# Kernel tuning notes

Measured on AMD Instinct MI355X. Metric: run time of the kernel, lower is better.

## Reference

```python
import jax, jax.numpy as jnp
import numpy as np

B, N, DIM = 2, 2048, 1024
H, DH = 16, 64
INNER = H * DH
SCALE = DH ** -0.5


def rotate_half(x):
    x1, x2 = jnp.split(x, 2, axis=-1)
    return jnp.concatenate((-x2, x1), axis=-1)


def apply_rotary(pos, t):
    # pos: [n, dh] broadcast against t: [b, h, n, dh]
    return t * jnp.cos(pos) + rotate_half(t) * jnp.sin(pos)


def setup_inputs() -> dict:
    key = jax.random.key(0)
    ks = jax.random.split(key, 5)
    x = jax.random.normal(ks[0], (B, N, DIM), dtype=jnp.float32)
    rotary_emb = jax.random.normal(ks[1], (N, DH), dtype=jnp.float32)
    w_qkv = jax.random.normal(ks[2], (3 * INNER, DIM), dtype=jnp.float32) * (DIM ** -0.5)
    w_out = jax.random.normal(ks[3], (DIM, INNER), dtype=jnp.float32) * (INNER ** -0.5)
    b_out = jax.random.normal(ks[4], (DIM,), dtype=jnp.float32) * 0.01
    return {"x": x, "rotary_emb": rotary_emb, "w_qkv": w_qkv, "w_out": w_out, "b_out": b_out}


def reference(x, rotary_emb, w_qkv, w_out, b_out):
    b, n, _ = x.shape
    qkv = jnp.einsum('bnd,ed->bne', x, w_qkv)  # [b, n, 3*inner]
    q, k, v = jnp.split(qkv, 3, axis=-1)
    # [b, n, inner] -> [b, h, n, dh]
    reshape = lambda t: t.reshape(b, n, H, DH).transpose(0, 2, 1, 3)
    q, k, v = reshape(q), reshape(k), reshape(v)
    q = apply_rotary(rotary_emb, q)
    k = apply_rotary(rotary_emb, k)
    dots = jnp.einsum('bhid,bhjd->bhij', q, k) * SCALE
    attn = jax.nn.softmax(dots, axis=-1)
    out = jnp.einsum('bhij,bhjd->bhid', attn, v)
    out = out.transpose(0, 2, 1, 3).reshape(b, n, INNER)
    return jnp.einsum('bne,de->bnd', out, w_out) + b_out
```

## Files before the change

### kernel.cpp

```cpp
#include <hip/hip_runtime.h>
#include <math.h>

typedef unsigned short ushort_t;
typedef __attribute__((ext_vector_type(8))) short short8v;
typedef __attribute__((ext_vector_type(4))) float float4v;

#define BB 2
#define NN 2048
#define HH 16
#define DHH 64
#define DIMM 1024
#define QKV3 3072
#define INNERR 1024
#define QSCALE 0.1803368801111244f

__device__ __forceinline__ ushort_t f2bf(float f) {
    unsigned u = __float_as_uint(f);
    u += 0x7fffu + ((u >> 16) & 1u);
    return (ushort_t)(u >> 16);
}
__device__ __forceinline__ float bf2f(unsigned h) {
    return __uint_as_float(h << 16);
}
__device__ __forceinline__ unsigned pk_bf16(float a, float b) {
#if __has_builtin(__builtin_amdgcn_cvt_pk_bf16_f32)
    typedef __attribute__((ext_vector_type(2))) __bf16 bf16x2;
    bf16x2 r = __builtin_amdgcn_cvt_pk_bf16_f32(a, b);
    return __builtin_bit_cast(unsigned, r);
#else
    return (unsigned)f2bf(a) | ((unsigned)f2bf(b) << 16);
#endif
}
__device__ __forceinline__ float fast_exp2(float x) {
#if __has_builtin(__builtin_amdgcn_exp2f)
    return __builtin_amdgcn_exp2f(x);
#else
    return exp2f(x);
#endif
}
__device__ __forceinline__ void gl2lds16(const void* g, void* l) {
    __builtin_amdgcn_global_load_lds(
        (const __attribute__((address_space(1))) unsigned int*)g,
        (__attribute__((address_space(3))) unsigned int*)l, 16, 0, 0);
}

__global__ __launch_bounds__(256) void conv_fused(const float* __restrict__ x,
                                                  const float* __restrict__ wqkv,
                                                  const float* __restrict__ wout,
                                                  ushort_t* __restrict__ xo,
                                                  ushort_t* __restrict__ wqkvo,
                                                  ushort_t* __restrict__ wouto) {
    int blk = blockIdx.x;
    const float* in; ushort_t* out; int i;
    if (blk < 4096)      { in = x;    out = xo;    i = blk * 256 + threadIdx.x; }
    else if (blk < 7168) { in = wqkv; out = wqkvo; i = (blk - 4096) * 256 + threadIdx.x; }
    else                 { in = wout; out = wouto; i = (blk - 7168) * 256 + threadIdx.x; }
    float4 v = ((const float4*)in)[i];
    ushort4 o;
    o.x = f2bf(v.x); o.y = f2bf(v.y); o.z = f2bf(v.z); o.w = f2bf(v.w);
    ((ushort4*)out)[i] = o;
}

template <int NOUT, bool BF16OUT, bool BIAS, bool ROT>
__global__ __launch_bounds__(256, 6) void gemm_bf16(const ushort_t* __restrict__ A,
                                                    const ushort_t* __restrict__ Bm,
                                                    const float* __restrict__ bias,
                                                    const float* __restrict__ rot,
                                                    ushort_t* __restrict__ Vt,
                                                    void* __restrict__ Cout, int K) {
    constexpr int NCH = 3;
    __shared__ ushort_t As[2][128 * 32];
    __shared__ ushort_t Bs[2][64 * 32];
    const int t = threadIdx.x;
    const int lane = t & 63;
    const int w = t >> 6;
    const int quad = lane >> 4;
    const int l15 = lane & 15;
    const int m0 = blockIdx.y * 128;
    const int n0 = blockIdx.x * 64;
    const int wm = w * 32;

    float4v acc[2][4];
#pragma unroll
    for (int i = 0; i < 2; ++i)
#pragma unroll
        for (int j = 0; j < 4; ++j) acc[i][j] = (float4v)0.0f;

    int srow[NCH], slc[NCH], sdst[NCH];
    bool sisA[NCH];
#pragma unroll
    for (int u = 0; u < NCH; ++u) {
        int c = u * 256 + t;
        if (c < 512) {
            int row = c >> 2;
            sisA[u] = true; srow[u] = row; slc[u] = (c & 3) ^ ((row >> 1) & 3); sdst[u] = c * 8;
        } else {
            int cb = c - 512;
            int row = cb >> 2;
            sisA[u] = false; srow[u] = row; slc[u] = (cb & 3) ^ ((row >> 1) & 3); sdst[u] = cb * 8;
        }
    }
#pragma unroll
    for (int u = 0; u < NCH; ++u) {
        if (sisA[u]) gl2lds16(&A[(size_t)(m0 + srow[u]) * K + slc[u] * 8], &As[0][sdst[u]]);
        else         gl2lds16(&Bm[(size_t)(n0 + srow[u]) * K + slc[u] * 8], &Bs[0][sdst[u]]);
    }
    const int NIT = K >> 5;
    for (int it = 0; it < NIT; ++it) {
        const int cur = it & 1;
        if (it + 1 < NIT) {
            const int nxt = cur ^ 1;
            const int kc = (it + 1) << 5;
#pragma unroll
            for (int u = 0; u < NCH; ++u) {
                if (sisA[u]) gl2lds16(&A[(size_t)(m0 + srow[u]) * K + kc + slc[u] * 8], &As[nxt][sdst[u]]);
                else         gl2lds16(&Bm[(size_t)(n0 + srow[u]) * K + kc + slc[u] * 8], &Bs[nxt][sdst[u]]);
            }
            asm volatile("s_waitcnt vmcnt(3)\n\ts_barrier" ::: "memory");
        } else {
            asm volatile("s_waitcnt vmcnt(0)\n\ts_barrier" ::: "memory");
        }
        short8v a[2], b[4];
#pragma unroll
        for (int i = 0; i < 2; ++i) {
            int row = wm + i * 16 + l15;
            int pc = quad ^ ((row >> 1) & 3);
            a[i] = *(const short8v*)&As[cur][row * 32 + pc * 8];
        }
#pragma unroll
        for (int j = 0; j < 4; ++j) {
            int row = j * 16 + l15;
            int pc = quad ^ ((row >> 1) & 3);
            b[j] = *(const short8v*)&Bs[cur][row * 32 + pc * 8];
        }
#pragma unroll
        for (int i = 0; i < 2; ++i)
#pragma unroll
            for (int j = 0; j < 4; ++j)
                acc[i][j] = __builtin_amdgcn_mfma_f32_16x16x32_bf16(a[i], b[j], acc[i][j], 0, 0, 0);
        asm volatile("s_barrier" ::: "memory");
    }
    const int region = ROT ? (n0 >> 10) : 0;
    if (ROT && region == 2) {
#pragma unroll
        for (int i = 0; i < 2; ++i) {
            int grow = m0 + wm + i * 16 + quad * 4;
            int bb = grow >> 11, nn_ = grow & (NN - 1);
            int tk = nn_ & 63;
            int tp = (tk & 32) | ((tk & 12) << 1) | ((tk & 16) >> 2);
            int nstore = (nn_ & ~63) | tp;
#pragma unroll
            for (int j = 0; j < 4; ++j) {
                int vcol = n0 + j * 16 + l15 - 2048;
                int hh = vcol >> 6, dh = vcol & 63;
                uint2 st;
                st.x = pk_bf16(acc[i][j][0], acc[i][j][1]);
                st.y = pk_bf16(acc[i][j][2], acc[i][j][3]);
                *(uint2*)&Vt[((size_t)(bb * HH + hh) * DHH + dh) * NN + nstore] = st;
            }
        }
        return;
    }
    if (ROT) {
        float scale = (region == 0) ? QSCALE : 1.0f;
#pragma unroll
        for (int i = 0; i < 2; ++i) {
#pragma unroll
            for (int r = 0; r < 4; ++r) {
                int n = (m0 + wm + i * 16 + quad * 4 + r) & (NN - 1);
#pragma unroll
                for (int jl = 0; jl < 2; ++jl) {
                    int dh = jl * 16 + l15;
                    float plo = rot[n * DHH + dh];
                    float phi = rot[n * DHH + dh + 32];
                    float lo = acc[i][jl][r], hi = acc[i][jl + 2][r];
                    acc[i][jl][r]     = (lo * __cosf(plo) - hi * __sinf(plo)) * scale;
                    acc[i][jl + 2][r] = (hi * __cosf(phi) + lo * __sinf(phi)) * scale;
                }
            }
        }
    }
#pragma unroll
    for (int i = 0; i < 2; ++i) {
        int grow = m0 + wm + i * 16 + quad * 4;
#pragma unroll
        for (int j = 0; j < 4; ++j) {
            int gcol = n0 + j * 16 + l15;
            float bv = BIAS ? bias[gcol] : 0.0f;
#pragma unroll
            for (int r = 0; r < 4; ++r) {
                float v = acc[i][j][r] + bv;
                if (BF16OUT)
                    ((ushort_t*)Cout)[(size_t)(grow + r) * NOUT + gcol] = f2bf(v);
                else
                    ((float*)Cout)[(size_t)(grow + r) * NOUT + gcol] = v;
            }
        }
    }
}

__global__ __launch_bounds__(256, 4) void flash_mfma(const ushort_t* __restrict__ qkv,
                                                     const ushort_t* __restrict__ Vt,
                                                     ushort_t* __restrict__ po,
                                                     float* __restrict__ lp) {
    __shared__ ushort_t smem[16384];
    ushort_t* Osc = smem;
    const int t = threadIdx.x;
    const int lane = t & 63;
    const int w = t >> 6;
    const int quad = lane >> 4;
    const int l15 = lane & 15;
    const int blk = blockIdx.x;
    const int slot = blk >> 3;
    const int ks = slot & 1;
    const int qt = (slot >> 1) & 15;
    const int bh = (blk & 7) * 4 + (slot >> 5);
    const int b = bh >> 4, h = bh & 15;
    const int n0 = qt * 128;

    short8v bq[2][2];
#pragma unroll
    for (int g = 0; g < 2; ++g) {
        size_t qb = (size_t)(b * NN + n0 + w * 32 + g * 16 + l15) * QKV3 + h * DHH + quad * 8;
        bq[g][0] = *(const short8v*)&qkv[qb];
        bq[g][1] = *(const short8v*)&qkv[qb + 32];
    }
    float4v o_acc[2][4];
    float4v l_acc[2];
#pragma unroll
    for (int g = 0; g < 2; ++g) {
        l_acc[g] = (float4v)0.0f;
#pragma unroll
        for (int nb = 0; nb < 4; ++nb) o_acc[g][nb] = (float4v)0.0f;
    }
    const short one_bf = (short)0x3F80;
    short8v ones8 = {one_bf, one_bf, one_bf, one_bf, one_bf, one_bf, one_bf, one_bf};

    const int s0 = t, s1 = 256 + t;
    const int r0 = s0 >> 3, lc0 = (s0 & 7) ^ (r0 & 7);
    const int r1 = s1 >> 3, lc1 = (s1 & 7) ^ (r1 & 7);
    const int koff0 = r0 * QKV3 + lc0 * 8, koff1 = r1 * QKV3 + lc1 * 8;
    const int voff0 = r0 * NN + lc0 * 8,   voff1 = r1 * NN + lc1 * 8;
    const ushort_t* kp = qkv + (size_t)b * NN * QKV3 + INNERR + h * DHH + (size_t)ks * 1024 * QKV3;
    const ushort_t* vp = Vt + (size_t)(b * HH + h) * DHH * NN + ks * 1024;

    {
        gl2lds16(kp + koff0, smem + 0 * 4096 + s0 * 8);
        gl2lds16(kp + koff1, smem + 0 * 4096 + s1 * 8);
        gl2lds16(vp + voff0, smem + 2 * 4096 + s0 * 8);
        gl2lds16(vp + voff1, smem + 2 * 4096 + s1 * 8);
    }
    for (int jt = 0; jt < 16; ++jt) {
        const int cur = jt & 1;
        if (jt < 15) {
            kp += 64 * QKV3;
            vp += 64;
            const int nxt = cur ^ 1;
            gl2lds16(kp + koff0, smem + nxt * 4096 + s0 * 8);
            gl2lds16(kp + koff1, smem + nxt * 4096 + s1 * 8);
            gl2lds16(vp + voff0, smem + (2 + nxt) * 4096 + s0 * 8);
            gl2lds16(vp + voff1, smem + (2 + nxt) * 4096 + s1 * 8);
            asm volatile("s_waitcnt vmcnt(4)\n\ts_barrier" ::: "memory");
        } else {
            asm volatile("s_waitcnt vmcnt(0)\n\ts_barrier" ::: "memory");
        }
        const ushort_t* Ksc = smem + cur * 4096;
        const ushort_t* Vtc = smem + (2 + cur) * 4096;
        float4v s_acc[2][4];
#pragma unroll
        for (int g = 0; g < 2; ++g)
#pragma unroll
            for (int nb = 0; nb < 4; ++nb) s_acc[g][nb] = (float4v)0.0f;
#pragma unroll
        for (int kb = 0; kb < 2; ++kb)
#pragma unroll
            for (int nb = 0; nb < 4; ++nb) {
                int row = nb * 16 + l15;
                int pc = (kb * 4 + quad) ^ (row & 7);
                short8v ak = *(const short8v*)&Ksc[row * 64 + pc * 8];
                s_acc[0][nb] = __builtin_amdgcn_mfma_f32_16x16x32_bf16(ak, bq[0][kb], s_acc[0][nb], 0, 0, 0);
                s_acc[1][nb] = __builtin_amdgcn_mfma_f32_16x16x32_bf16(ak, bq[1][kb], s_acc[1][nb], 0, 0, 0);
            }
#pragma unroll
        for (int g = 0; g < 2; ++g) {
            float p[4][4];
#pragma unroll
            for (int nb = 0; nb < 4; ++nb)
#pragma unroll
                for (int r = 0; r < 4; ++r) p[nb][r] = fast_exp2(s_acc[g][nb][r]);
            uint4 u0, u1;
            u0.x = pk_bf16(p[0][0], p[0][1]); u0.y = pk_bf16(p[0][2], p[0][3]);
            u0.z = pk_bf16(p[1][0], p[1][1]); u0.w = pk_bf16(p[1][2], p[1][3]);
            u1.x = pk_bf16(p[2][0], p[2][1]); u1.y = pk_bf16(p[2][2], p[2][3]);
            u1.z = pk_bf16(p[3][0], p[3][1]); u1.w = pk_bf16(p[3][2], p[3][3]);
            short8v ap0 = __builtin_bit_cast(short8v, u0);
            short8v ap1 = __builtin_bit_cast(short8v, u1);
            l_acc[g] = __builtin_amdgcn_mfma_f32_16x16x32_bf16(ap0, ones8, l_acc[g], 0, 0, 0);
            l_acc[g] = __builtin_amdgcn_mfma_f32_16x16x32_bf16(ap1, ones8, l_acc[g], 0, 0, 0);
#pragma unroll
            for (int nb = 0; nb < 4; ++nb) {
                int row = nb * 16 + l15;
                int pc0 = quad ^ (row & 7);
                int pc1 = (4 + quad) ^ (row & 7);
                short8v bv0 = *(const short8v*)&Vtc[row * 64 + pc0 * 8];
                short8v bv1 = *(const short8v*)&Vtc[row * 64 + pc1 * 8];
                o_acc[g][nb] = __builtin_amdgcn_mfma_f32_16x16x32_bf16(ap0, bv0, o_acc[g][nb], 0, 0, 0);
                o_acc[g][nb] = __builtin_amdgcn_mfma_f32_16x16x32_bf16(ap1, bv1, o_acc[g][nb], 0, 0, 0);
            }
        }
        asm volatile("s_barrier" ::: "memory");
    }
#pragma unroll
    for (int g = 0; g < 2; ++g) {
        if (l15 == 0)
            *(float4*)&lp[(size_t)(ks * 32 + bh) * NN + n0 + w * 32 + g * 16 + quad * 4] =
                *(float4*)&l_acc[g];
    }
    ushort_t* osc = Osc + w * (32 * 68);
#pragma unroll
    for (int g = 0; g < 2; ++g)
#pragma unroll
        for (int nb = 0; nb < 4; ++nb)
#pragma unroll
            for (int r = 0; r < 4; ++r)
                osc[(g * 16 + quad * 4 + r) * 68 + nb * 16 + l15] = f2bf(o_acc[g][nb][r]);
    __builtin_amdgcn_s_waitcnt(0);
    {
        int rr = lane >> 1, c0 = (lane & 1) * 32;
        size_t prow = ((size_t)(ks * 32 + bh) * NN + n0 + w * 32 + rr) * DHH + c0;
#pragma unroll
        for (int u = 0; u < 4; ++u) {
            uint4 v = *(const uint4*)&osc[rr * 68 + c0 + u * 8];
            *(uint4*)&po[prow + u * 8] = v;
        }
    }
}

__global__ __launch_bounds__(256) void reduce_o(const ushort_t* __restrict__ po,
                                                const float* __restrict__ lp,
                                                ushort_t* __restrict__ attn) {
    int tg = blockIdx.x * 256 + threadIdx.x;
    int bh = tg >> 15;
    int rem = tg & 32767;
    int n = rem >> 4;
    int dh0 = (rem & 15) * 4;
    size_t p0 = ((size_t)bh * NN + n) * DHH + dh0;
    size_t p1 = p0 + (size_t)32 * NN * DHH;
    uint2 a = *(const uint2*)&po[p0];
    uint2 c = *(const uint2*)&po[p1];
    float inv = 1.0f / (lp[(size_t)bh * NN + n] + lp[(size_t)(32 + bh) * NN + n]);
    float o0 = (bf2f(a.x & 0xffff) + bf2f(c.x & 0xffff)) * inv;
    float o1 = (bf2f(a.x >> 16)    + bf2f(c.x >> 16))    * inv;
    float o2 = (bf2f(a.y & 0xffff) + bf2f(c.y & 0xffff)) * inv;
    float o3 = (bf2f(a.y >> 16)    + bf2f(c.y >> 16))    * inv;
    int b = bh >> 4, h = bh & 15;
    uint2 st;
    st.x = pk_bf16(o0, o1);
    st.y = pk_bf16(o2, o3);
    *(uint2*)&attn[((size_t)(b * NN + n)) * INNERR + h * DHH + dh0] = st;
}

extern "C" void kernel_launch(void* const* d_in, const int* in_sizes, int n_in,
                              void* d_out, int out_size, void* d_ws, size_t ws_size,
                              hipStream_t stream) {
    const float* x = (const float*)d_in[0];
    const float* rot = (const float*)d_in[1];
    const float* w_qkv = (const float*)d_in[2];
    const float* w_out = (const float*)d_in[3];
    const float* b_out = (const float*)d_in[4];
    float* y = (float*)d_out;

    char* ws = (char*)d_ws;
    ushort_t* qkv_bf  = (ushort_t*)(ws);
    ushort_t* vt_bf   = (ushort_t*)(ws + 25165824);
    ushort_t* wout_bf = (ushort_t*)(ws + 33554432);
    ushort_t* wqkv_bf = (ushort_t*)(ws + 35651584);
    float*    lp      = (float*)(ws + 35651584);
    ushort_t* x_bf    = (ushort_t*)(ws + 41943040);
    ushort_t* attn_bf = x_bf;
    ushort_t* po      = (ushort_t*)(ws + 50331648);

    conv_fused<<<8192, 256, 0, stream>>>(x, w_qkv, w_out, x_bf, wqkv_bf, wout_bf);
    gemm_bf16<QKV3, true, false, true><<<dim3(48, 32), 256, 0, stream>>>(
        x_bf, wqkv_bf, nullptr, rot, vt_bf, qkv_bf, DIMM);
    flash_mfma<<<1024, 256, 0, stream>>>(qkv_bf, vt_bf, po, lp);
    reduce_o<<<4096, 256, 0, stream>>>(po, lp, attn_bf);
    gemm_bf16<INNERR, false, true, false><<<dim3(16, 32), 256, 0, stream>>>(
        attn_bf, wout_bf, b_out, nullptr, nullptr, y, INNERR);
}
```

Measured before the change: 201.3 us.

## Add block-index swizzle and smaller 64-row tile for output projection GEMM

Makes the GEMM template take the tile height and a swizzle width. The grid becomes 1D, and block indices are remapped so that groups of blocks share N tiles, which is meant to improve L2 reuse. The output projection now uses 64x64 tiles with a 2x2 warp layout, giving 1024 blocks instead of 512 for better occupancy across CUs. The cost is smaller per-block MFMA work and more redundant A/B loads for that GEMM.

After: 202.4 us. About the same (+0.6%).

```diff
diff --git a/kernel.cpp b/kernel.cpp
--- a/kernel.cpp
+++ b/kernel.cpp
@@ -61,41 +61,46 @@
     ((ushort4*)out)[i] = o;
 }
 
-template <int NOUT, bool BF16OUT, bool BIAS, bool ROT>
+template <int NOUT, bool BF16OUT, bool BIAS, bool ROT, int BM, int SWXN>
 __global__ __launch_bounds__(256, 6) void gemm_bf16(const ushort_t* __restrict__ A,
                                                     const ushort_t* __restrict__ Bm,
                                                     const float* __restrict__ bias,
                                                     const float* __restrict__ rot,
                                                     ushort_t* __restrict__ Vt,
                                                     void* __restrict__ Cout, int K) {
-    constexpr int NCH = 3;
-    __shared__ ushort_t As[2][128 * 32];
+    constexpr int JN = (BM == 128) ? 4 : 2;
+    constexpr int ACH = BM * 4;
+    constexpr int NCH = (ACH + 256) / 256;
+    __shared__ ushort_t As[2][BM * 32];
     __shared__ ushort_t Bs[2][64 * 32];
     const int t = threadIdx.x;
     const int lane = t & 63;
     const int w = t >> 6;
     const int quad = lane >> 4;
     const int l15 = lane & 15;
-    const int m0 = blockIdx.y * 128;
-    const int n0 = blockIdx.x * 64;
-    const int wm = w * 32;
-
-    float4v acc[2][4];
+    const int blk = blockIdx.x;
+    const int ii = blk >> 3;
+    const int m0 = (ii / SWXN) * BM;
+    const int n0 = ((blk & 7) * SWXN + ii % SWXN) * 64;
+    const int wm = (BM == 128) ? w * 32 : (w >> 1) * 32;
+    const int wn = (BM == 128) ? 0 : (w & 1) * 32;
+
+    float4v acc[2][JN];
 #pragma unroll
     for (int i = 0; i < 2; ++i)
 #pragma unroll
-        for (int j = 0; j < 4; ++j) acc[i][j] = (float4v)0.0f;
+        for (int j = 0; j < JN; ++j) acc[i][j] = (float4v)0.0f;
 
     int srow[NCH], slc[NCH], sdst[NCH];
     bool sisA[NCH];
 #pragma unroll
     for (int u = 0; u < NCH; ++u) {
         int c = u * 256 + t;
-        if (c < 512) {
+        if (c < ACH) {
             int row = c >> 2;
             sisA[u] = true; srow[u] = row; slc[u] = (c & 3) ^ ((row >> 1) & 3); sdst[u] = c * 8;
         } else {
-            int cb = c - 512;
+            int cb = c - ACH;
             int row = cb >> 2;
             sisA[u] = false; srow[u] = row; slc[u] = (cb & 3) ^ ((row >> 1) & 3); sdst[u] = cb * 8;
         }
@@ -116,11 +121,12 @@
                 if (sisA[u]) gl2lds16(&A[(size_t)(m0 + srow[u]) * K + kc + slc[u] * 8], &As[nxt][sdst[u]]);
                 else         gl2lds16(&Bm[(size_t)(n0 + srow[u]) * K + kc + slc[u] * 8], &Bs[nxt][sdst[u]]);
             }
-            asm volatile("s_waitcnt vmcnt(3)\n\ts_barrier" ::: "memory");
+            if (NCH == 3) asm volatile("s_waitcnt vmcnt(3)\n\ts_barrier" ::: "memory");
+            else          asm volatile("s_waitcnt vmcnt(2)\n\ts_barrier" ::: "memory");
         } else {
             asm volatile("s_waitcnt vmcnt(0)\n\ts_barrier" ::: "memory");
         }
-        short8v a[2], b[4];
+        short8v a[2], b[JN];
 #pragma unroll
         for (int i = 0; i < 2; ++i) {
             int row = wm + i * 16 + l15;
@@ -128,15 +134,15 @@
             a[i] = *(const short8v*)&As[cur][row * 32 + pc * 8];
         }
 #pragma unroll
-        for (int j = 0; j < 4; ++j) {
-            int row = j * 16 + l15;
+        for (int j = 0; j < JN; ++j) {
+            int row = wn + j * 16 + l15;
             int pc = quad ^ ((row >> 1) & 3);
             b[j] = *(const short8v*)&Bs[cur][row * 32 + pc * 8];
         }
 #pragma unroll
         for (int i = 0; i < 2; ++i)
 #pragma unroll
-            for (int j = 0; j < 4; ++j)
+            for (int j = 0; j < JN; ++j)
                 acc[i][j] = __builtin_amdgcn_mfma_f32_16x16x32_bf16(a[i], b[j], acc[i][j], 0, 0, 0);
         asm volatile("s_barrier" ::: "memory");
     }
@@ -150,7 +156,7 @@
             int tp = (tk & 32) | ((tk & 12) << 1) | ((tk & 16) >> 2);
             int nstore = (nn_ & ~63) | tp;
 #pragma unroll
-            for (int j = 0; j < 4; ++j) {
+            for (int j = 0; j < JN; ++j) {
                 int vcol = n0 + j * 16 + l15 - 2048;
                 int hh = vcol >> 6, dh = vcol & 63;
                 uint2 st;
@@ -184,8 +190,8 @@
     for (int i = 0; i < 2; ++i) {
         int grow = m0 + wm + i * 16 + quad * 4;
 #pragma unroll
-        for (int j = 0; j < 4; ++j) {
-            int gcol = n0 + j * 16 + l15;
+        for (int j = 0; j < JN; ++j) {
+            int gcol = n0 + wn + j * 16 + l15;
             float bv = BIAS ? bias[gcol] : 0.0f;
 #pragma unroll
             for (int r = 0; r < 4; ++r) {
@@ -381,10 +387,10 @@
     ushort_t* po      = (ushort_t*)(ws + 50331648);
 
     conv_fused<<<8192, 256, 0, stream>>>(x, w_qkv, w_out, x_bf, wqkv_bf, wout_bf);
-    gemm_bf16<QKV3, true, false, true><<<dim3(48, 32), 256, 0, stream>>>(
+    gemm_bf16<QKV3, true, false, true, 128, 6><<<1536, 256, 0, stream>>>(
         x_bf, wqkv_bf, nullptr, rot, vt_bf, qkv_bf, DIMM);
     flash_mfma<<<1024, 256, 0, stream>>>(qkv_bf, vt_bf, po, lp);
     reduce_o<<<4096, 256, 0, stream>>>(po, lp, attn_bf);
-    gemm_bf16<INNERR, false, true, false><<<dim3(16, 32), 256, 0, stream>>>(
+    gemm_bf16<INNERR, false, true, false, 64, 2><<<1024, 256, 0, stream>>>(
         attn_bf, wout_bf, b_out, nullptr, nullptr, y, INNERR);
 }
```

## Fuse split-KV reduction into output GEMM and remap block tiles

Applied to the files above, without the earlier changes.

Removes the separate reduce_o kernel by having a new output-projection GEMM load both split-KV partial outputs and row sums, then normalize and convert them to bf16 while staging A tiles into shared memory. The output GEMM also moves to 64x64 tiles with 1024 blocks instead of 128x64 with 512 blocks. The QKV GEMM becomes a specialized kernel with a 1D grid that groups blocks across N columns, aiming for better L2 reuse. This saves one launch and an intermediate write and read, but adds redundant reduction work, since each A element is recombined for every N-tile, and uses a smaller tile for the final GEMM.

New measurement: 209.0 us. 3.9% more time.

```diff
diff --git a/kernel.cpp b/kernel.cpp
--- a/kernel.cpp
+++ b/kernel.cpp
@@ -61,13 +61,13 @@
     ((ushort4*)out)[i] = o;
 }
 
-template <int NOUT, bool BF16OUT, bool BIAS, bool ROT>
-__global__ __launch_bounds__(256, 6) void gemm_bf16(const ushort_t* __restrict__ A,
+template <int SWXN>
+__global__ __launch_bounds__(256, 6) void gemm1_qkv(const ushort_t* __restrict__ A,
                                                     const ushort_t* __restrict__ Bm,
-                                                    const float* __restrict__ bias,
                                                     const float* __restrict__ rot,
                                                     ushort_t* __restrict__ Vt,
-                                                    void* __restrict__ Cout, int K) {
+                                                    ushort_t* __restrict__ Cout) {
+    constexpr int K = DIMM;
     constexpr int NCH = 3;
     __shared__ ushort_t As[2][128 * 32];
     __shared__ ushort_t Bs[2][64 * 32];
@@ -76,8 +76,10 @@
     const int w = t >> 6;
     const int quad = lane >> 4;
     const int l15 = lane & 15;
-    const int m0 = blockIdx.y * 128;
-    const int n0 = blockIdx.x * 64;
+    const int blk = blockIdx.x;
+    const int ii = blk >> 3;
+    const int m0 = (ii / SWXN) * 128;
+    const int n0 = ((blk & 7) * SWXN + ii % SWXN) * 64;
     const int wm = w * 32;
 
     float4v acc[2][4];
@@ -140,8 +142,8 @@
                 acc[i][j] = __builtin_amdgcn_mfma_f32_16x16x32_bf16(a[i], b[j], acc[i][j], 0, 0, 0);
         asm volatile("s_barrier" ::: "memory");
     }
-    const int region = ROT ? (n0 >> 10) : 0;
-    if (ROT && region == 2) {
+    const int region = n0 >> 10;
+    if (region == 2) {
 #pragma unroll
         for (int i = 0; i < 2; ++i) {
             int grow = m0 + wm + i * 16 + quad * 4;
@@ -161,22 +163,20 @@
         }
         return;
     }
-    if (ROT) {
-        float scale = (region == 0) ? QSCALE : 1.0f;
-#pragma unroll
-        for (int i = 0; i < 2; ++i) {
-#pragma unroll
-            for (int r = 0; r < 4; ++r) {
-                int n = (m0 + wm + i * 16 + quad * 4 + r) & (NN - 1);
-#pragma unroll
-                for (int jl = 0; jl < 2; ++jl) {
-                    int dh = jl * 16 + l15;
-                    float plo = rot[n * DHH + dh];
-                    float phi = rot[n * DHH + dh + 32];
-                    float lo = acc[i][jl][r], hi = acc[i][jl + 2][r];
-                    acc[i][jl][r]     = (lo * __cosf(plo) - hi * __sinf(plo)) * scale;
-                    acc[i][jl + 2][r] = (hi * __cosf(phi) + lo * __sinf(phi)) * scale;
-                }
+    float scale = (region == 0) ? QSCALE : 1.0f;
+#pragma unroll
+    for (int i = 0; i < 2; ++i) {
+#pragma unroll
+        for (int r = 0; r < 4; ++r) {
+            int n = (m0 + wm + i * 16 + quad * 4 + r) & (NN - 1);
+#pragma unroll
+            for (int jl = 0; jl < 2; ++jl) {
+                int dh = jl * 16 + l15;
+                float plo = rot[n * DHH + dh];
+                float phi = rot[n * DHH + dh + 32];
+                float lo = acc[i][jl][r], hi = acc[i][jl + 2][r];
+                acc[i][jl][r]     = (lo * __cosf(plo) - hi * __sinf(plo)) * scale;
+                acc[i][jl + 2][r] = (hi * __cosf(phi) + lo * __sinf(phi)) * scale;
             }
         }
     }
@@ -186,15 +186,122 @@
 #pragma unroll
         for (int j = 0; j < 4; ++j) {
             int gcol = n0 + j * 16 + l15;
-            float bv = BIAS ? bias[gcol] : 0.0f;
-#pragma unroll
-            for (int r = 0; r < 4; ++r) {
-                float v = acc[i][j][r] + bv;
-                if (BF16OUT)
-                    ((ushort_t*)Cout)[(size_t)(grow + r) * NOUT + gcol] = f2bf(v);
-                else
-                    ((float*)Cout)[(size_t)(grow + r) * NOUT + gcol] = v;
-            }
+#pragma unroll
+            for (int r = 0; r < 4; ++r)
+                Cout[(size_t)(grow + r) * QKV3 + gcol] = f2bf(acc[i][j][r]);
+        }
+    }
+}
+
+__global__ __launch_bounds__(256, 6) void gemm2_fused(const ushort_t* __restrict__ po,
+                                                      const float* __restrict__ lp,
+                                                      const ushort_t* __restrict__ Bm,
+                                                      const float* __restrict__ bias,
+                                                      float* __restrict__ y) {
+    __shared__ ushort_t As[2][64 * 32];
+    __shared__ ushort_t Bs[2][64 * 32];
+    const int t = threadIdx.x;
+    const int lane = t & 63;
+    const int w = t >> 6;
+    const int quad = lane >> 4;
+    const int l15 = lane & 15;
+    const int blk = blockIdx.x;
+    const int ii = blk >> 3;
+    const int m0 = (ii / 2) * 64;
+    const int n0 = ((blk & 7) * 2 + ii % 2) * 64;
+    const int wm = (w >> 1) * 32;
+    const int wn = (w & 1) * 32;
+
+    float4v acc[2][2];
+#pragma unroll
+    for (int i = 0; i < 2; ++i)
+#pragma unroll
+        for (int j = 0; j < 2; ++j) acc[i][j] = (float4v)0.0f;
+
+    const int r = t >> 2;
+    const int slcA = (t & 3) ^ ((r >> 1) & 3);
+    const int tok = m0 + r;
+    const int bb = tok >> 11, nn_ = tok & (NN - 1);
+    const size_t lpb = (size_t)(bb * 16) * NN + nn_;
+
+    union U8 { uint4 v; unsigned u[4]; };
+    U8 pa0, pa1, bw;
+    float lv0, lv1;
+    {
+        size_t pbase = ((size_t)(bb * 16) * NN + nn_) * DHH + slcA * 8;
+        pa0.v = *(const uint4*)&po[pbase];
+        pa1.v = *(const uint4*)&po[pbase + (size_t)32 * NN * DHH];
+        lv0 = lp[lpb];
+        lv1 = lp[lpb + (size_t)32 * NN];
+        bw.v = *(const uint4*)&Bm[(size_t)(n0 + r) * INNERR + slcA * 8];
+        float inv = 1.0f / (lv0 + lv1);
+        uint4 st;
+#pragma unroll
+        for (int q2 = 0; q2 < 4; ++q2) {
+            float e0 = (bf2f(pa0.u[q2] & 0xffff) + bf2f(pa1.u[q2] & 0xffff)) * inv;
+            float e1 = (bf2f(pa0.u[q2] >> 16)    + bf2f(pa1.u[q2] >> 16))    * inv;
+            ((unsigned*)&st)[q2] = pk_bf16(e0, e1);
+        }
+        *(uint4*)&As[0][t * 8] = st;
+        *(uint4*)&Bs[0][t * 8] = bw.v;
+    }
+    const int NIT = INNERR >> 5;
+    for (int it = 0; it < NIT; ++it) {
+        const int cur = it & 1;
+        asm volatile("s_waitcnt lgkmcnt(0)\n\ts_barrier" ::: "memory");
+        short8v a[2], b[2];
+#pragma unroll
+        for (int i = 0; i < 2; ++i) {
+            int row = wm + i * 16 + l15;
+            int pc = quad ^ ((row >> 1) & 3);
+            a[i] = *(const short8v*)&As[cur][row * 32 + pc * 8];
+        }
+#pragma unroll
+        for (int j = 0; j < 2; ++j) {
+            int row = wn + j * 16 + l15;
+            int pc = quad ^ ((row >> 1) & 3);
+            b[j] = *(const short8v*)&Bs[cur][row * 32 + pc * 8];
+        }
+        if (it + 1 < NIT) {
+            const int kc = (it + 1) << 5;
+            const int h = kc >> 6;
+            const int dh0 = (kc & 63 & 32) + slcA * 8;
+            size_t pbase = ((size_t)(bb * 16 + h) * NN + nn_) * DHH + dh0;
+            pa0.v = *(const uint4*)&po[pbase];
+            pa1.v = *(const uint4*)&po[pbase + (size_t)32 * NN * DHH];
+            lv0 = lp[lpb + (size_t)h * NN];
+            lv1 = lp[lpb + (size_t)(32 + h) * NN];
+            bw.v = *(const uint4*)&Bm[(size_t)(n0 + r) * INNERR + kc + slcA * 8];
+        }
+#pragma unroll
+        for (int i = 0; i < 2; ++i)
+#pragma unroll
+            for (int j = 0; j < 2; ++j)
+                acc[i][j] = __builtin_amdgcn_mfma_f32_16x16x32_bf16(a[i], b[j], acc[i][j], 0, 0, 0);
+        if (it + 1 < NIT) {
+            const int nxt = cur ^ 1;
+            float inv = 1.0f / (lv0 + lv1);
+            uint4 st;
+#pragma unroll
+            for (int q2 = 0; q2 < 4; ++q2) {
+                float e0 = (bf2f(pa0.u[q2] & 0xffff) + bf2f(pa1.u[q2] & 0xffff)) * inv;
+                float e1 = (bf2f(pa0.u[q2] >> 16)    + bf2f(pa1.u[q2] >> 16))    * inv;
+                ((unsigned*)&st)[q2] = pk_bf16(e0, e1);
+            }
+            *(uint4*)&As[nxt][t * 8] = st;
+            *(uint4*)&Bs[nxt][t * 8] = bw.v;
+        }
+    }
+#pragma unroll
+    for (int i = 0; i < 2; ++i) {
+        int grow = m0 + wm + i * 16 + quad * 4;
+#pragma unroll
+        for (int j = 0; j < 2; ++j) {
+            int gcol = n0 + wn + j * 16 + l15;
+            float bv = bias[gcol];
+#pragma unroll
+            for (int rr = 0; rr < 4; ++rr)
+                y[(size_t)(grow + rr) * INNERR + gcol] = acc[i][j][rr] + bv;
         }
     }
 }
@@ -287,7 +394,7 @@
 #pragma unroll
             for (int nb = 0; nb < 4; ++nb)
 #pragma unroll
-                for (int r = 0; r < 4; ++r) p[nb][r] = fast_exp2(s_acc[g][nb][r]);
+                for (int rr = 0; rr < 4; ++rr) p[nb][rr] = fast_exp2(s_acc[g][nb][rr]);
             uint4 u0, u1;
             u0.x = pk_bf16(p[0][0], p[0][1]); u0.y = pk_bf16(p[0][2], p[0][3]);
             u0.z = pk_bf16(p[1][0], p[1][1]); u0.w = pk_bf16(p[1][2], p[1][3]);
@@ -322,8 +429,8 @@
 #pragma unroll
         for (int nb = 0; nb < 4; ++nb)
 #pragma unroll
-            for (int r = 0; r < 4; ++r)
-                osc[(g * 16 + quad * 4 + r) * 68 + nb * 16 + l15] = f2bf(o_acc[g][nb][r]);
+            for (int rr = 0; rr < 4; ++rr)
+                osc[(g * 16 + quad * 4 + rr) * 68 + nb * 16 + l15] = f2bf(o_acc[g][nb][rr]);
     __builtin_amdgcn_s_waitcnt(0);
     {
         int rr = lane >> 1, c0 = (lane & 1) * 32;
@@ -334,30 +441,6 @@
             *(uint4*)&po[prow + u * 8] = v;
         }
     }
-}
-
-__global__ __launch_bounds__(256) void reduce_o(const ushort_t* __restrict__ po,
-                                                const float* __restrict__ lp,
-                                                ushort_t* __restrict__ attn) {
-    int tg = blockIdx.x * 256 + threadIdx.x;
-    int bh = tg >> 15;
-    int rem = tg & 32767;
-    int n = rem >> 4;
-    int dh0 = (rem & 15) * 4;
-    size_t p0 = ((size_t)bh * NN + n) * DHH + dh0;
-    size_t p1 = p0 + (size_t)32 * NN * DHH;
-    uint2 a = *(const uint2*)&po[p0];
-    uint2 c = *(const uint2*)&po[p1];
-    float inv = 1.0f / (lp[(size_t)bh * NN + n] + lp[(size_t)(32 + bh) * NN + n]);
-    float o0 = (bf2f(a.x & 0xffff) + bf2f(c.x & 0xffff)) * inv;
-    float o1 = (bf2f(a.x >> 16)    + bf2f(c.x >> 16))    * inv;
-    float o2 = (bf2f(a.y & 0xffff) + bf2f(c.y & 0xffff)) * inv;
-    float o3 = (bf2f(a.y >> 16)    + bf2f(c.y >> 16))    * inv;
-    int b = bh >> 4, h = bh & 15;
-    uint2 st;
-    st.x = pk_bf16(o0, o1);
-    st.y = pk_bf16(o2, o3);
-    *(uint2*)&attn[((size_t)(b * NN + n)) * INNERR + h * DHH + dh0] = st;
 }
 
 extern "C" void kernel_launch(void* const* d_in, const int* in_sizes, int n_in,
@@ -377,14 +460,10 @@
     ushort_t* wqkv_bf = (ushort_t*)(ws + 35651584);
     float*    lp      = (float*)(ws + 35651584);
     ushort_t* x_bf    = (ushort_t*)(ws + 41943040);
-    ushort_t* attn_bf = x_bf;
     ushort_t* po      = (ushort_t*)(ws + 50331648);
 
     conv_fused<<<8192, 256, 0, stream>>>(x, w_qkv, w_out, x_bf, wqkv_bf, wout_bf);
-    gemm_bf16<QKV3, true, false, true><<<dim3(48, 32), 256, 0, stream>>>(
-        x_bf, wqkv_bf, nullptr, rot, vt_bf, qkv_bf, DIMM);
+    gemm1_qkv<6><<<1536, 256, 0, stream>>>(x_bf, wqkv_bf, rot, vt_bf, qkv_bf);
     flash_mfma<<<1024, 256, 0, stream>>>(qkv_bf, vt_bf, po, lp);
-    reduce_o<<<4096, 256, 0, stream>>>(po, lp, attn_bf);
-    gemm_bf16<INNERR, false, true, false><<<dim3(16, 32), 256, 0, stream>>>(
-        attn_bf, wout_bf, b_out, nullptr, nullptr, y, INNERR);
-}
+    gemm2_fused<<<1024, 256, 0, stream>>>(po, lp, wout_bf, b_out, y);
+}
```
